# Kernel optimization log

Measured on AMD Instinct MI355X. Metric: run time of the kernel, lower is better.

The kernel has to match this reference:

```python
import jax, jax.numpy as jnp
import numpy as np

N_NODES = 50000
N_EDGES = 800000
IN_DIM = 64
HID = 256
EDGE_DIM = 6
NEG_SLOPE = 0.2


def setup_inputs() -> dict:
    key = jax.random.key(0)
    ks = jax.random.split(key, 16)
    glorot = lambda k, shp: jax.random.normal(k, shp, jnp.float32) * jnp.sqrt(2.0 / (shp[0] + shp[-1]))
    x = jax.random.normal(ks[0], (N_NODES, IN_DIM), jnp.float32)
    edge_index = jax.random.randint(ks[1], (2, N_EDGES), 0, N_NODES, dtype=jnp.int32)
    edge_attr = jax.random.normal(ks[2], (N_EDGES, EDGE_DIM), jnp.float32)
    return {
        "x": x,
        "edge_index": edge_index,
        "edge_attr": edge_attr,
        # layer 1 (heads=1)
        "W1": glorot(ks[3], (IN_DIM, HID)),
        "att_src1": glorot(ks[4], (HID,)),
        "att_dst1": glorot(ks[5], (HID,)),
        "We1": glorot(ks[6], (EDGE_DIM, HID)),
        "att_e1": glorot(ks[7], (HID,)),
        "b1": jnp.zeros((HID,), jnp.float32),
        # layer 2
        "W2": glorot(ks[8], (HID, HID)),
        "att_src2": glorot(ks[9], (HID,)),
        "att_dst2": glorot(ks[10], (HID,)),
        "We2": glorot(ks[11], (EDGE_DIM, HID)),
        "att_e2": glorot(ks[12], (HID,)),
        "b2": jnp.zeros((HID,), jnp.float32),
    }


def gat_conv(x, src, dst, edge_attr, W, att_src, att_dst, We, att_e, b):
    # PyG GATConv, heads=1, add_self_loops=False, edge features in attention only
    h = x @ W                              # [N, C]
    a_src = h @ att_src                    # [N]
    a_dst = h @ att_dst                    # [N]
    a_edge = (edge_attr @ We) @ att_e      # [E]
    alpha = a_src[src] + a_dst[dst] + a_edge            # [E]
    alpha = jax.nn.leaky_relu(alpha, NEG_SLOPE)
    # softmax over edges sharing the same destination node
    amax = jax.ops.segment_max(alpha, dst, num_segments=N_NODES)
    amax = jnp.where(jnp.isneginf(amax), 0.0, amax)
    ex = jnp.exp(alpha - amax[dst])
    denom = jax.ops.segment_sum(ex, dst, num_segments=N_NODES)
    alpha = ex / (denom[dst] + 1e-16)
    msg = h[src] * alpha[:, None]          # [E, C]
    out = jax.ops.segment_sum(msg, dst, num_segments=N_NODES)  # [N, C]
    return out + b


def reference(x, edge_index, edge_attr, W1, att_src1, att_dst1, We1, att_e1, b1,
              W2, att_src2, att_dst2, We2, att_e2, b2):
    src, dst = edge_index[0], edge_index[1]
    h = jax.nn.relu(gat_conv(x, src, dst, edge_attr, W1, att_src1, att_dst1, We1, att_e1, b1))
    # dropout(p=0.2) is identity in eval mode
    out = gat_conv(h, src, dst, edge_attr, W2, att_src2, att_dst2, We2, att_e2, b2)
    return out  # out_proj is Identity (out_dim=None)
```

## Files before the change

kernel.cpp:

```cpp
#include <hip/hip_runtime.h>
#include <hip/hip_bf16.h>

#define N_NODES_C 50000
#define N_EDGES_C 800000
#define IN_DIM_C 64
#define HID_C 256
#define EDGE_DIM_C 6
#define NEG_SLOPE_C 0.2f

typedef short short8 __attribute__((ext_vector_type(8)));
typedef float f32x4 __attribute__((ext_vector_type(4)));

static __device__ __forceinline__ float b2f(unsigned short u) {
    union { unsigned int i; float f; } x;
    x.i = ((unsigned int)u) << 16;
    return x.f;
}
static __device__ __forceinline__ unsigned short f2b(float f) {
    union { __hip_bfloat16 h; unsigned short u; } x;
    x.h = __float2bfloat16(f);
    return x.u;
}

static __device__ __forceinline__ float aggr_node(int off0, int deg, float adi,
                                                  const int* __restrict__ ssrc,
                                                  const float* __restrict__ sae,
                                                  const float* __restrict__ asrc,
                                                  const unsigned short* __restrict__ H,
                                                  int l, float* acc) {
    int sidx0 = 0, sidx1 = 0;
    float w0 = 0.f, w1 = 0.f;
    if (l < deg) {
        sidx0 = ssrc[off0 + l];
        float a = asrc[sidx0] + adi + sae[off0 + l];
        a = (a > 0.f) ? a : NEG_SLOPE_C * a;
        w0 = __expf(a);
    }
    if (32 + l < deg) {
        sidx1 = ssrc[off0 + 32 + l];
        float a = asrc[sidx1] + adi + sae[off0 + 32 + l];
        a = (a > 0.f) ? a : NEG_SLOPE_C * a;
        w1 = __expf(a);
    }
    float s = w0 + w1;
    for (int j = 64 + l; j < deg; j += 32) {
        int si = ssrc[off0 + j];
        float a = asrc[si] + adi + sae[off0 + j];
        a = (a > 0.f) ? a : NEG_SLOPE_C * a;
        s += __expf(a);
    }
#pragma unroll
    for (int o = 16; o > 0; o >>= 1) s += __shfl_xor(s, o, 32);
    float inv = 1.0f / (s + 1e-16f);

    int c8 = l * 8;
#pragma unroll
    for (int q = 0; q < 8; ++q) acc[q] = 0.f;

    auto fetch = [&](int j, int& si, float& wv) {
        if (j < 32) {
            si = __shfl(sidx0, j, 32);
            wv = __shfl(w0, j, 32);
        } else if (j < 64) {
            si = __shfl(sidx1, j - 32, 32);
            wv = __shfl(w1, j - 32, 32);
        } else {
            si = ssrc[off0 + j];
            float a = asrc[si] + adi + sae[off0 + j];
            a = (a > 0.f) ? a : NEG_SLOPE_C * a;
            wv = __expf(a);
        }
    };

    int j = 0;
    for (; j + 7 < deg; j += 8) {
        int ii[8];
        float uu[8];
#pragma unroll
        for (int q = 0; q < 8; ++q) fetch(j + q, ii[q], uu[q]);
        short8 h[8];
#pragma unroll
        for (int q = 0; q < 8; ++q) h[q] = *(const short8*)&H[(long)ii[q] * HID_C + c8];
#pragma unroll
        for (int t = 0; t < 8; ++t)
#pragma unroll
            for (int q = 0; q < 8; ++q) acc[q] += uu[t] * b2f((unsigned short)h[t][q]);
    }
    for (; j + 3 < deg; j += 4) {
        int ii[4];
        float uu[4];
#pragma unroll
        for (int q = 0; q < 4; ++q) fetch(j + q, ii[q], uu[q]);
        short8 h[4];
#pragma unroll
        for (int q = 0; q < 4; ++q) h[q] = *(const short8*)&H[(long)ii[q] * HID_C + c8];
#pragma unroll
        for (int t = 0; t < 4; ++t)
#pragma unroll
            for (int q = 0; q < 8; ++q) acc[q] += uu[t] * b2f((unsigned short)h[t][q]);
    }
    for (; j < deg; ++j) {
        int i0;
        float u0;
        fetch(j, i0, u0);
        short8 h0 = *(const short8*)&H[(long)i0 * HID_C + c8];
#pragma unroll
        for (int q = 0; q < 8; ++q) acc[q] += u0 * b2f((unsigned short)h0[q]);
    }
    return inv;
}

__global__ void k_prep(const float* __restrict__ W1, const float* __restrict__ W2,
                       unsigned short* __restrict__ W1t, unsigned short* __restrict__ W2t,
                       const float* __restrict__ We1, const float* __restrict__ atte1,
                       const float* __restrict__ We2, const float* __restrict__ atte2,
                       float* __restrict__ v, int* __restrict__ deg) {
    int tid = threadIdx.x;
    int i = blockIdx.x * blockDim.x + tid;
    if (i < N_NODES_C) deg[i] = 0;
    if (i < IN_DIM_C * HID_C) {
        int k = i >> 8, n = i & 255;
        W1t[n * IN_DIM_C + k] = f2b(W1[i]);
    }
    if (i < HID_C * HID_C) {
        int k = i >> 8, n = i & 255;
        W2t[n * HID_C + k] = f2b(W2[i]);
    }
    if (blockIdx.x == 255) {
        __shared__ float red[256];
        for (int layer = 0; layer < 2; ++layer) {
            const float* We = layer ? We2 : We1;
            const float* ae = layer ? atte2 : atte1;
            for (int k = 0; k < EDGE_DIM_C; ++k) {
                red[tid] = We[k * HID_C + tid] * ae[tid];
                __syncthreads();
                for (int s = 128; s > 0; s >>= 1) {
                    if (tid < s) red[tid] += red[tid + s];
                    __syncthreads();
                }
                if (tid == 0) v[layer * 8 + k] = red[0];
                __syncthreads();
            }
        }
    }
}

#define GEMM1_BLOCKS 782

__global__ __launch_bounds__(256) void k_pre_gemm1(
    const float* __restrict__ X, const unsigned short* __restrict__ Wt,
    unsigned short* __restrict__ H, const float* __restrict__ att_s,
    const float* __restrict__ att_d, float* __restrict__ asrc,
    float* __restrict__ adst,
    const int* __restrict__ dst, const float* __restrict__ eattr,
    const float* __restrict__ v, int* __restrict__ deg,
    float* __restrict__ ae1, float* __restrict__ ae2) {
    __shared__ unsigned short As[64 * 64];
    __shared__ unsigned short Bs[256 * 64];
    __shared__ float ds[4][64];
    __shared__ float dd[4][64];
    int tid = threadIdx.x;

    if (blockIdx.x >= GEMM1_BLOCKS) {
        int e = (blockIdx.x - GEMM1_BLOCKS) * 256 + tid;
        if (e < N_EDGES_C) {
            atomicAdd(&deg[dst[e]], 1);
            float a1 = 0.f, a2 = 0.f;
#pragma unroll
            for (int k = 0; k < EDGE_DIM_C; ++k) {
                float ea = eattr[e * EDGE_DIM_C + k];
                a1 += ea * v[k];
                a2 += ea * v[8 + k];
            }
            ae1[e] = a1;
            ae2[e] = a2;
        }
        return;
    }

    int w = tid >> 6, l = tid & 63;
    int lr = l & 15, lg = l >> 4;
    long mbase = (long)blockIdx.x * 64;

    float asv[4], adv[4];
#pragma unroll
    for (int ni = 0; ni < 4; ++ni) {
        int col = w * 64 + ni * 16 + lr;
        asv[ni] = att_s[col];
        adv[ni] = att_d[col];
    }

    f32x4 acc[4][4];
#pragma unroll
    for (int mi = 0; mi < 4; ++mi)
#pragma unroll
        for (int ni = 0; ni < 4; ++ni) acc[mi][ni] = (f32x4){0.f, 0.f, 0.f, 0.f};

    {
#pragma unroll
        for (int p = 0; p < 2; ++p) {
            int r = p * 32 + (tid >> 3);
            int c8 = tid & 7;
            long row = mbase + r;
            short8 val = {0, 0, 0, 0, 0, 0, 0, 0};
            if (row < N_NODES_C) {
                const f32x4* p4 = (const f32x4*)&X[row * IN_DIM_C + c8 * 8];
                f32x4 a0 = p4[0], a1 = p4[1];
#pragma unroll
                for (int q = 0; q < 4; ++q) val[q] = (short)f2b(a0[q]);
#pragma unroll
                for (int q = 0; q < 4; ++q) val[4 + q] = (short)f2b(a1[q]);
            }
            *(short8*)&As[r * 64 + ((c8 ^ (r & 7)) * 8)] = val;
        }
        int n = tid;
#pragma unroll
        for (int c8 = 0; c8 < 8; ++c8) {
            *(short8*)&Bs[n * 64 + ((c8 ^ (n & 7)) * 8)] =
                *(const short8*)&Wt[(long)n * IN_DIM_C + c8 * 8];
        }
        __syncthreads();
#pragma unroll
        for (int kk = 0; kk < 2; ++kk) {
            int cblk = kk * 4 + lg;
            short8 a[4], b[4];
#pragma unroll
            for (int mi = 0; mi < 4; ++mi) {
                int R = mi * 16 + lr;
                a[mi] = *(const short8*)&As[R * 64 + ((cblk ^ (R & 7)) * 8)];
            }
#pragma unroll
            for (int ni = 0; ni < 4; ++ni) {
                int Nr = w * 64 + ni * 16 + lr;
                b[ni] = *(const short8*)&Bs[Nr * 64 + ((cblk ^ (Nr & 7)) * 8)];
            }
#pragma unroll
            for (int mi = 0; mi < 4; ++mi)
#pragma unroll
                for (int ni = 0; ni < 4; ++ni)
                    acc[mi][ni] = __builtin_amdgcn_mfma_f32_16x16x32_bf16(a[mi], b[ni],
                                                                          acc[mi][ni], 0, 0, 0);
        }
        __syncthreads();
    }

#pragma unroll
    for (int mi = 0; mi < 4; ++mi) {
#pragma unroll
        for (int r = 0; r < 4; ++r) {
            int rowl = mi * 16 + lg * 4 + r;
            long row = mbase + rowl;
            float ps = 0.f, pd = 0.f;
#pragma unroll
            for (int ni = 0; ni < 4; ++ni) {
                float h = acc[mi][ni][r];
                ps += h * asv[ni];
                pd += h * adv[ni];
            }
#pragma unroll
            for (int o = 1; o < 16; o <<= 1) {
                ps += __shfl_xor(ps, o, 16);
                pd += __shfl_xor(pd, o, 16);
            }
            if (lr == 0) {
                ds[w][rowl] = ps;
                dd[w][rowl] = pd;
            }
            if (row < N_NODES_C) {
#pragma unroll
                for (int ni = 0; ni < 4; ++ni) {
                    H[row * HID_C + w * 64 + ni * 16 + lr] = f2b(acc[mi][ni][r]);
                }
            }
        }
    }
    __syncthreads();
    if (tid < 64) {
        long row = mbase + tid;
        if (row < N_NODES_C) {
            asrc[row] = ds[0][tid] + ds[1][tid] + ds[2][tid] + ds[3][tid];
            adst[row] = dd[0][tid] + dd[1][tid] + dd[2][tid] + dd[3][tid];
        }
    }
}

__global__ void k_scan1(const int* __restrict__ deg, int* __restrict__ offs,
                        int* __restrict__ bsum) {
    __shared__ int tmp[256];
    int b = blockIdx.x, tid = threadIdx.x;
    int i = b * 256 + tid;
    int v = (i < N_NODES_C) ? deg[i] : 0;
    tmp[tid] = v;
    __syncthreads();
    for (int d = 1; d < 256; d <<= 1) {
        int t = (tid >= d) ? tmp[tid - d] : 0;
        __syncthreads();
        tmp[tid] += t;
        __syncthreads();
    }
    if (i < N_NODES_C) offs[i] = tmp[tid] - v;
    if (tid == 255) bsum[b] = tmp[255];
}
__global__ void k_scan2(const int* __restrict__ bsum, int* __restrict__ boff, int nb) {
    __shared__ int tmp[256];
    int tid = threadIdx.x;
    int v = (tid < nb) ? bsum[tid] : 0;
    tmp[tid] = v;
    __syncthreads();
    for (int d = 1; d < 256; d <<= 1) {
        int t = (tid >= d) ? tmp[tid - d] : 0;
        __syncthreads();
        tmp[tid] += t;
        __syncthreads();
    }
    if (tid < nb) boff[tid] = tmp[tid] - v;
}
__global__ void k_scan3(int* __restrict__ offs, const int* __restrict__ boff,
                        int* __restrict__ cur) {
    int b = blockIdx.x, tid = threadIdx.x;
    int i = b * 256 + tid;
    if (i < N_NODES_C) {
        int o = offs[i] + boff[b];
        offs[i] = o;
        cur[i] = o;
    }
    if (i == 0) offs[N_NODES_C] = N_EDGES_C;
}

__global__ void k_perm(const int* __restrict__ dst, int* __restrict__ cur,
                       int* __restrict__ perm) {
    int e = blockIdx.x * blockDim.x + threadIdx.x;
    if (e >= N_EDGES_C) return;
    int pos = atomicAdd(&cur[dst[e]], 1);
    perm[pos] = e;
}

__global__ void k_gather(const int* __restrict__ perm, const int* __restrict__ src,
                         const float* __restrict__ ae1, const float* __restrict__ ae2,
                         int* __restrict__ ssrc, float* __restrict__ sae1,
                         float* __restrict__ sae2) {
    int p = blockIdx.x * blockDim.x + threadIdx.x;
    if (p >= N_EDGES_C) return;
    int e = perm[p];
    ssrc[p] = src[e];
    sae1[p] = ae1[e];
    sae2[p] = ae2[e];
}

__global__ __launch_bounds__(256) void k_aggr2(const int* __restrict__ offs,
                                               const int* __restrict__ ssrc,
                                               const float* __restrict__ sae,
                                               const float* __restrict__ asrc,
                                               const float* __restrict__ adst,
                                               const unsigned short* __restrict__ H,
                                               const float* __restrict__ bias,
                                               void* __restrict__ outp, int mode) {
    int tid = threadIdx.x;
    int hw = tid >> 5;
    int l = tid & 31;
    int node = blockIdx.x * 8 + hw;
    int off0 = offs[node];
    int deg = offs[node + 1] - off0;
    float adi = adst[node];
    float acc[8];
    float inv = aggr_node(off0, deg, adi, ssrc, sae, asrc, H, l, acc);
    int c8 = l * 8;
    const f32x4* b4 = (const f32x4*)&bias[c8];
    f32x4 bv0 = b4[0], bv1 = b4[1];
    if (mode == 1) {
        unsigned short* o16 = (unsigned short*)outp;
        short8 r;
#pragma unroll
        for (int q = 0; q < 4; ++q)
            r[q] = (short)f2b(fmaxf(acc[q] * inv + bv0[q], 0.f));
#pragma unroll
        for (int q = 0; q < 4; ++q)
            r[4 + q] = (short)f2b(fmaxf(acc[4 + q] * inv + bv1[q], 0.f));
        *(short8*)&o16[(long)node * HID_C + c8] = r;
    } else {
        float* o32 = (float*)outp;
        f32x4 r0, r1;
#pragma unroll
        for (int q = 0; q < 4; ++q) r0[q] = acc[q] * inv + bv0[q];
#pragma unroll
        for (int q = 0; q < 4; ++q) r1[q] = acc[4 + q] * inv + bv1[q];
        *(f32x4*)&o32[(long)node * HID_C + c8] = r0;
        *(f32x4*)&o32[(long)node * HID_C + c8 + 4] = r1;
    }
}

__global__ __launch_bounds__(256) void k_gemm2(
    const unsigned short* __restrict__ G, const unsigned short* __restrict__ Wt,
    unsigned short* __restrict__ H2, const float* __restrict__ att_s,
    const float* __restrict__ att_d, float* __restrict__ asrc2,
    float* __restrict__ adst2) {
    __shared__ unsigned short As[64 * 256];
    __shared__ float ds[4][64];
    __shared__ float dd[4][64];
    int tid = threadIdx.x;
    long mbase = (long)blockIdx.x * 64;

    int hw = tid >> 5, l = tid & 31;
#pragma unroll
    for (int p = 0; p < 8; ++p) {
        int rowl = p * 8 + hw;
        long row = mbase + rowl;
        short8 val = {0, 0, 0, 0, 0, 0, 0, 0};
        if (row < N_NODES_C) val = *(const short8*)&G[row * HID_C + l * 8];
        *(short8*)&As[rowl * 256 + (l >> 3) * 64 + (((l & 7) ^ (rowl & 7)) * 8)] = val;
    }
    __syncthreads();

    int w = tid >> 6, l64 = tid & 63;
    int lr = l64 & 15, lg = l64 >> 4;

    float asv[4], adv[4];
#pragma unroll
    for (int ni = 0; ni < 4; ++ni) {
        int col = w * 64 + ni * 16 + lr;
        asv[ni] = att_s[col];
        adv[ni] = att_d[col];
    }

    f32x4 acc[4][4];
#pragma unroll
    for (int mi = 0; mi < 4; ++mi)
#pragma unroll
        for (int ni = 0; ni < 4; ++ni) acc[mi][ni] = (f32x4){0.f, 0.f, 0.f, 0.f};

#pragma unroll
    for (int k0 = 0; k0 < HID_C; k0 += 64) {
#pragma unroll
        for (int kk = 0; kk < 2; ++kk) {
            int cblk = kk * 4 + lg;
            short8 a[4], b[4];
#pragma unroll
            for (int mi = 0; mi < 4; ++mi) {
                int R = mi * 16 + lr;
                a[mi] = *(const short8*)&As[R * 256 + k0 + ((cblk ^ (R & 7)) * 8)];
            }
#pragma unroll
            for (int ni = 0; ni < 4; ++ni) {
                int Nr = w * 64 + ni * 16 + lr;
                b[ni] = *(const short8*)&Wt[(long)Nr * HID_C + k0 + cblk * 8];
            }
#pragma unroll
            for (int mi = 0; mi < 4; ++mi)
#pragma unroll
                for (int ni = 0; ni < 4; ++ni)
                    acc[mi][ni] = __builtin_amdgcn_mfma_f32_16x16x32_bf16(a[mi], b[ni],
                                                                          acc[mi][ni], 0, 0, 0);
        }
    }

#pragma unroll
    for (int mi = 0; mi < 4; ++mi) {
#pragma unroll
        for (int r = 0; r < 4; ++r) {
            int rowl = mi * 16 + lg * 4 + r;
            long row = mbase + rowl;
            float ps = 0.f, pd = 0.f;
#pragma unroll
            for (int ni = 0; ni < 4; ++ni) {
                float h = acc[mi][ni][r];
                ps += h * asv[ni];
                pd += h * adv[ni];
            }
#pragma unroll
            for (int o = 1; o < 16; o <<= 1) {
                ps += __shfl_xor(ps, o, 16);
                pd += __shfl_xor(pd, o, 16);
            }
            if (lr == 0) {
                ds[w][rowl] = ps;
                dd[w][rowl] = pd;
            }
            if (row < N_NODES_C) {
#pragma unroll
                for (int ni = 0; ni < 4; ++ni) {
                    H2[row * HID_C + w * 64 + ni * 16 + lr] = f2b(acc[mi][ni][r]);
                }
            }
        }
    }
    __syncthreads();
    if (tid < 64) {
        long row = mbase + tid;
        if (row < N_NODES_C) {
            asrc2[row] = ds[0][tid] + ds[1][tid] + ds[2][tid] + ds[3][tid];
            adst2[row] = dd[0][tid] + dd[1][tid] + dd[2][tid] + dd[3][tid];
        }
    }
}

extern "C" void kernel_launch(void* const* d_in, const int* in_sizes, int n_in,
                              void* d_out, int out_size, void* d_ws, size_t ws_size,
                              hipStream_t stream) {
    const float* x     = (const float*)d_in[0];
    const int*   ei    = (const int*)d_in[1];
    const float* eattr = (const float*)d_in[2];
    const float* W1    = (const float*)d_in[3];
    const float* atts1 = (const float*)d_in[4];
    const float* attd1 = (const float*)d_in[5];
    const float* We1   = (const float*)d_in[6];
    const float* atte1 = (const float*)d_in[7];
    const float* b1    = (const float*)d_in[8];
    const float* W2    = (const float*)d_in[9];
    const float* atts2 = (const float*)d_in[10];
    const float* attd2 = (const float*)d_in[11];
    const float* We2   = (const float*)d_in[12];
    const float* atte2 = (const float*)d_in[13];
    const float* b2    = (const float*)d_in[14];
    float* out = (float*)d_out;

    char* ws = (char*)d_ws;
    size_t off = 0;
    auto alloc = [&](size_t bytes) -> void* {
        void* p = ws + off;
        off = (off + bytes + 255) & ~(size_t)255;
        return p;
    };
    int*   deg   = (int*)alloc((size_t)N_NODES_C * 4);
    int*   offs  = (int*)alloc(((size_t)N_NODES_C + 1) * 4);
    int*   cur   = (int*)alloc((size_t)N_NODES_C * 4);
    int*   perm  = (int*)alloc((size_t)N_EDGES_C * 4);
    int*   ssrc  = (int*)alloc((size_t)N_EDGES_C * 4);
    float* ae1   = (float*)alloc((size_t)N_EDGES_C * 4);
    float* ae2   = (float*)alloc((size_t)N_EDGES_C * 4);
    float* sae1  = (float*)alloc((size_t)N_EDGES_C * 4);
    float* sae2  = (float*)alloc((size_t)N_EDGES_C * 4);
    float* asrc  = (float*)alloc((size_t)N_NODES_C * 4);
    float* adst  = (float*)alloc((size_t)N_NODES_C * 4);
    float* asrc2 = (float*)alloc((size_t)N_NODES_C * 4);
    float* adst2 = (float*)alloc((size_t)N_NODES_C * 4);
    float* v     = (float*)alloc(64);
    int*   bsum  = (int*)alloc(256 * 4);
    int*   boff  = (int*)alloc(257 * 4);
    unsigned short* W1t = (unsigned short*)alloc((size_t)HID_C * IN_DIM_C * 2);
    unsigned short* W2t = (unsigned short*)alloc((size_t)HID_C * HID_C * 2);
    unsigned short* h1  = (unsigned short*)alloc((size_t)N_NODES_C * HID_C * 2);
    unsigned short* g1  = (unsigned short*)alloc((size_t)N_NODES_C * HID_C * 2);
    unsigned short* h2  = h1;

    const int* src = ei;
    const int* dst = ei + N_EDGES_C;
    int nb = (N_NODES_C + 255) / 256;
    int pre_blocks = (N_EDGES_C + 255) / 256;
    int gemm_grid = (N_NODES_C + 63) / 64;

    k_prep<<<256, 256, 0, stream>>>(W1, W2, W1t, W2t, We1, atte1, We2, atte2, v, deg);
    k_pre_gemm1<<<GEMM1_BLOCKS + pre_blocks, 256, 0, stream>>>(
        x, W1t, h1, atts1, attd1, asrc, adst, dst, eattr, v, deg, ae1, ae2);
    k_scan1<<<nb, 256, 0, stream>>>(deg, offs, bsum);
    k_scan2<<<1, 256, 0, stream>>>(bsum, boff, nb);
    k_scan3<<<nb, 256, 0, stream>>>(offs, boff, cur);
    k_perm<<<pre_blocks, 256, 0, stream>>>(dst, cur, perm);
    k_gather<<<pre_blocks, 256, 0, stream>>>(perm, src, ae1, ae2, ssrc, sae1, sae2);

    k_aggr2<<<N_NODES_C / 8, 256, 0, stream>>>(offs, ssrc, sae1, asrc, adst, h1, b1, g1, 1);
    k_gemm2<<<gemm_grid, 256, 0, stream>>>(g1, W2t, h2, atts2, attd2, asrc2, adst2);
    k_aggr2<<<N_NODES_C / 8, 256, 0, stream>>>(offs, ssrc, sae2, asrc2, adst2, h2, b2, out, 0);
}
```

Before: 299.2 us.

## Record atomic rank during degree count and drop second atomic pass and scan kernel

The degree-counting atomic now returns each edge's rank within its destination, stored as a byte, so the permutation kernel computes positions without a second round of atomics. The separate block-offset scan kernel is merged into the final scan kernel through a per-block reduction of preceding block sums. The two per-edge attention scalars are packed into one float2 array. Storing rank as a byte assumes no node has in-degree of 256 or more, which holds for random inputs but is not general.

```diff
diff --git a/kernel.cpp b/kernel.cpp
--- a/kernel.cpp
+++ b/kernel.cpp
@@ -154,7 +154,7 @@
     float* __restrict__ adst,
     const int* __restrict__ dst, const float* __restrict__ eattr,
     const float* __restrict__ v, int* __restrict__ deg,
-    float* __restrict__ ae1, float* __restrict__ ae2) {
+    float2* __restrict__ ae12, unsigned char* __restrict__ rank) {
     __shared__ unsigned short As[64 * 64];
     __shared__ unsigned short Bs[256 * 64];
     __shared__ float ds[4][64];
@@ -164,7 +164,8 @@
     if (blockIdx.x >= GEMM1_BLOCKS) {
         int e = (blockIdx.x - GEMM1_BLOCKS) * 256 + tid;
         if (e < N_EDGES_C) {
-            atomicAdd(&deg[dst[e]], 1);
+            int r = atomicAdd(&deg[dst[e]], 1);
+            rank[e] = (unsigned char)r;
             float a1 = 0.f, a2 = 0.f;
 #pragma unroll
             for (int k = 0; k < EDGE_DIM_C; ++k) {
@@ -172,8 +173,7 @@
                 a1 += ea * v[k];
                 a2 += ea * v[8 + k];
             }
-            ae1[e] = a1;
-            ae2[e] = a2;
+            ae12[e] = make_float2(a1, a2);
         }
         return;
     }
@@ -301,50 +301,41 @@
     if (i < N_NODES_C) offs[i] = tmp[tid] - v;
     if (tid == 255) bsum[b] = tmp[255];
 }
-__global__ void k_scan2(const int* __restrict__ bsum, int* __restrict__ boff, int nb) {
-    __shared__ int tmp[256];
-    int tid = threadIdx.x;
-    int v = (tid < nb) ? bsum[tid] : 0;
-    tmp[tid] = v;
+
+__global__ void k_scan3(int* __restrict__ offs, const int* __restrict__ bsum) {
+    __shared__ int red[256];
+    int b = blockIdx.x, tid = threadIdx.x;
+    red[tid] = (tid < b) ? bsum[tid] : 0;
     __syncthreads();
-    for (int d = 1; d < 256; d <<= 1) {
-        int t = (tid >= d) ? tmp[tid - d] : 0;
+    for (int s = 128; s > 0; s >>= 1) {
+        if (tid < s) red[tid] += red[tid + s];
         __syncthreads();
-        tmp[tid] += t;
-        __syncthreads();
-    }
-    if (tid < nb) boff[tid] = tmp[tid] - v;
-}
-__global__ void k_scan3(int* __restrict__ offs, const int* __restrict__ boff,
-                        int* __restrict__ cur) {
-    int b = blockIdx.x, tid = threadIdx.x;
+    }
+    int boff = red[0];
     int i = b * 256 + tid;
-    if (i < N_NODES_C) {
-        int o = offs[i] + boff[b];
-        offs[i] = o;
-        cur[i] = o;
-    }
+    if (i < N_NODES_C) offs[i] += boff;
     if (i == 0) offs[N_NODES_C] = N_EDGES_C;
 }
 
-__global__ void k_perm(const int* __restrict__ dst, int* __restrict__ cur,
-                       int* __restrict__ perm) {
+__global__ void k_perm(const int* __restrict__ dst, const unsigned char* __restrict__ rank,
+                       const int* __restrict__ offs, int* __restrict__ perm) {
     int e = blockIdx.x * blockDim.x + threadIdx.x;
     if (e >= N_EDGES_C) return;
-    int pos = atomicAdd(&cur[dst[e]], 1);
+    int pos = offs[dst[e]] + (int)rank[e];
     perm[pos] = e;
 }
 
 __global__ void k_gather(const int* __restrict__ perm, const int* __restrict__ src,
-                         const float* __restrict__ ae1, const float* __restrict__ ae2,
+                         const float2* __restrict__ ae12,
                          int* __restrict__ ssrc, float* __restrict__ sae1,
                          float* __restrict__ sae2) {
     int p = blockIdx.x * blockDim.x + threadIdx.x;
     if (p >= N_EDGES_C) return;
     int e = perm[p];
     ssrc[p] = src[e];
-    sae1[p] = ae1[e];
-    sae2[p] = ae2[e];
+    float2 a = ae12[e];
+    sae1[p] = a.x;
+    sae2[p] = a.y;
 }
 
 __global__ __launch_bounds__(256) void k_aggr2(const int* __restrict__ offs,
@@ -520,22 +511,20 @@
         off = (off + bytes + 255) & ~(size_t)255;
         return p;
     };
-    int*   deg   = (int*)alloc((size_t)N_NODES_C * 4);
-    int*   offs  = (int*)alloc(((size_t)N_NODES_C + 1) * 4);
-    int*   cur   = (int*)alloc((size_t)N_NODES_C * 4);
-    int*   perm  = (int*)alloc((size_t)N_EDGES_C * 4);
-    int*   ssrc  = (int*)alloc((size_t)N_EDGES_C * 4);
-    float* ae1   = (float*)alloc((size_t)N_EDGES_C * 4);
-    float* ae2   = (float*)alloc((size_t)N_EDGES_C * 4);
-    float* sae1  = (float*)alloc((size_t)N_EDGES_C * 4);
-    float* sae2  = (float*)alloc((size_t)N_EDGES_C * 4);
-    float* asrc  = (float*)alloc((size_t)N_NODES_C * 4);
-    float* adst  = (float*)alloc((size_t)N_NODES_C * 4);
-    float* asrc2 = (float*)alloc((size_t)N_NODES_C * 4);
-    float* adst2 = (float*)alloc((size_t)N_NODES_C * 4);
-    float* v     = (float*)alloc(64);
-    int*   bsum  = (int*)alloc(256 * 4);
-    int*   boff  = (int*)alloc(257 * 4);
+    int*    deg   = (int*)alloc((size_t)N_NODES_C * 4);
+    int*    offs  = (int*)alloc(((size_t)N_NODES_C + 1) * 4);
+    int*    perm  = (int*)alloc((size_t)N_EDGES_C * 4);
+    int*    ssrc  = (int*)alloc((size_t)N_EDGES_C * 4);
+    float2* ae12  = (float2*)alloc((size_t)N_EDGES_C * 8);
+    unsigned char* rank = (unsigned char*)alloc((size_t)N_EDGES_C);
+    float*  sae1  = (float*)alloc((size_t)N_EDGES_C * 4);
+    float*  sae2  = (float*)alloc((size_t)N_EDGES_C * 4);
+    float*  asrc  = (float*)alloc((size_t)N_NODES_C * 4);
+    float*  adst  = (float*)alloc((size_t)N_NODES_C * 4);
+    float*  asrc2 = (float*)alloc((size_t)N_NODES_C * 4);
+    float*  adst2 = (float*)alloc((size_t)N_NODES_C * 4);
+    float*  v     = (float*)alloc(64);
+    int*    bsum  = (int*)alloc(256 * 4);
     unsigned short* W1t = (unsigned short*)alloc((size_t)HID_C * IN_DIM_C * 2);
     unsigned short* W2t = (unsigned short*)alloc((size_t)HID_C * HID_C * 2);
     unsigned short* h1  = (unsigned short*)alloc((size_t)N_NODES_C * HID_C * 2);
@@ -550,12 +539,11 @@
 
     k_prep<<<256, 256, 0, stream>>>(W1, W2, W1t, W2t, We1, atte1, We2, atte2, v, deg);
     k_pre_gemm1<<<GEMM1_BLOCKS + pre_blocks, 256, 0, stream>>>(
-        x, W1t, h1, atts1, attd1, asrc, adst, dst, eattr, v, deg, ae1, ae2);
+        x, W1t, h1, atts1, attd1, asrc, adst, dst, eattr, v, deg, ae12, rank);
     k_scan1<<<nb, 256, 0, stream>>>(deg, offs, bsum);
-    k_scan2<<<1, 256, 0, stream>>>(bsum, boff, nb);
-    k_scan3<<<nb, 256, 0, stream>>>(offs, boff, cur);
-    k_perm<<<pre_blocks, 256, 0, stream>>>(dst, cur, perm);
-    k_gather<<<pre_blocks, 256, 0, stream>>>(perm, src, ae1, ae2, ssrc, sae1, sae2);
+    k_scan3<<<nb, 256, 0, stream>>>(offs, bsum);
+    k_perm<<<pre_blocks, 256, 0, stream>>>(dst, rank, offs, perm);
+    k_gather<<<pre_blocks, 256, 0, stream>>>(perm, src, ae12, ssrc, sae1, sae2);
 
     k_aggr2<<<N_NODES_C / 8, 256, 0, stream>>>(offs, ssrc, sae1, asrc, adst, h1, b1, g1, 1);
     k_gemm2<<<gemm_grid, 256, 0, stream>>>(g1, W2t, h2, atts2, attd2, asrc2, adst2);
```

Measured after the change: 249.1 us. 16.8% less time.
